# Optimization experiments

Hardware: AMD Instinct MI355X
Metric: run time of the kernel (lower is better)

Reference implementation:

```python
import math
import jax, jax.numpy as jnp
import numpy as np

N, L, D, H = 2, 2048, 1024, 16
DK = D // H  # 64


def setup_inputs() -> dict:
    key = jax.random.key(0)
    k1, k2, k3, k4, k5 = jax.random.split(key, 5)
    scale = 1.0 / math.sqrt(D)
    return {
        "values": jax.random.normal(k1, (N, L, D), dtype=jnp.float32),
        "keys": jax.random.normal(k2, (N, L, D), dtype=jnp.float32),
        "queries": jax.random.normal(k3, (N, L, D), dtype=jnp.float32),
        "fc_out_w": jax.random.normal(k4, (D, D), dtype=jnp.float32) * scale,
        "fc_out_b": jax.random.normal(k5, (D,), dtype=jnp.float32) * scale,
    }


def reference(values, keys, queries, fc_out_w, fc_out_b):
    n, q_len, _ = queries.shape
    k_len = keys.shape[1]
    v = values.reshape(n, k_len, H, DK)
    k = keys.reshape(n, k_len, H, DK)
    q = queries.reshape(n, q_len, H, DK)
    # NOTE: the original module never applies its per-head Linear layers (dead code),
    # and scales logits AFTER the QK einsum.
    energy = jnp.einsum('nqhd,nkhd->nhqk', q, k)  # [N,H,q,k]
    p_attn = jax.nn.softmax(energy / math.sqrt(DK), axis=3)
    attn = jnp.einsum('nhqk,nkhd->nqhd', p_attn, v).reshape(n, q_len, H * DK)
    # fc_out: torch Linear -> x @ W.T + b
    return attn @ fc_out_w.T + fc_out_b
```

## Files before the change

kernel.cpp:

```cpp
#include <hip/hip_runtime.h>
#include <hip/hip_bf16.h>

#define NBATCH 2
#define SEQ    2048
#define DMODEL 1024
#define NHEAD  16
#define DHEAD  64
#define NHTOT  (NBATCH*NHEAD)

typedef __attribute__((ext_vector_type(8)))  short          short8;
typedef __attribute__((ext_vector_type(4)))  float          f32x4;
typedef __attribute__((ext_vector_type(16))) float          f32x16;
typedef __attribute__((ext_vector_type(4)))  unsigned short ushort4v;

__device__ __forceinline__ unsigned short f2bf(float x) {
  union { __hip_bfloat16 b; unsigned short u; } c;
  c.b = __float2bfloat16(x);
  return c.u;
}

__device__ __forceinline__ unsigned int cvt_pk_bf16(float lo, float hi) {
  unsigned int r;
  asm("v_cvt_pk_bf16_f32 %0, %1, %2" : "=v"(r) : "v"(lo), "v"(hi));
  return r;
}

__device__ __forceinline__ void gl_lds16(const unsigned short* g, unsigned short* l) {
  __builtin_amdgcn_global_load_lds(
      (const __attribute__((address_space(1))) void*)g,
      (__attribute__((address_space(3))) void*)l, 16, 0, 0);
}

__global__ __launch_bounds__(256) void cvt_qk(const float* __restrict__ q,
                                              const float* __restrict__ k,
                                              unsigned short* __restrict__ qb,
                                              unsigned short* __restrict__ kb) {
  const float QSCALE = 0.125f * 1.44269504088896340736f;
  int e = (blockIdx.x * 256 + threadIdx.x) * 8;
  int n = e >> 21;
  int r = e & ((1 << 21) - 1);
  int l = r >> 10;
  int c = r & 1023;
  int h = c >> 6;
  int d = c & 63;
  size_t dst = ((size_t)(n * NHEAD + h) * SEQ + l) * DHEAD + d;
  float4 q0 = *reinterpret_cast<const float4*>(q + e);
  float4 q1 = *reinterpret_cast<const float4*>(q + e + 4);
  float4 k0 = *reinterpret_cast<const float4*>(k + e);
  float4 k1 = *reinterpret_cast<const float4*>(k + e + 4);
  union { unsigned short u[8]; short8 s; } qo, ko;
  qo.u[0]=f2bf(q0.x*QSCALE); qo.u[1]=f2bf(q0.y*QSCALE);
  qo.u[2]=f2bf(q0.z*QSCALE); qo.u[3]=f2bf(q0.w*QSCALE);
  qo.u[4]=f2bf(q1.x*QSCALE); qo.u[5]=f2bf(q1.y*QSCALE);
  qo.u[6]=f2bf(q1.z*QSCALE); qo.u[7]=f2bf(q1.w*QSCALE);
  ko.u[0]=f2bf(k0.x); ko.u[1]=f2bf(k0.y); ko.u[2]=f2bf(k0.z); ko.u[3]=f2bf(k0.w);
  ko.u[4]=f2bf(k1.x); ko.u[5]=f2bf(k1.y); ko.u[6]=f2bf(k1.z); ko.u[7]=f2bf(k1.w);
  *reinterpret_cast<short8*>(qb + dst) = qo.s;
  *reinterpret_cast<short8*>(kb + dst) = ko.s;
}

__global__ __launch_bounds__(256) void vtrans(const float* __restrict__ v,
                                              unsigned short* __restrict__ vt) {
  __shared__ __align__(16) unsigned short t[64][76];
  int bid = blockIdx.x;
  int nh = bid >> 5;
  int lt = bid & 31;
  int n = nh >> 4, h = nh & 15;
  int lbase = lt * 64;
  #pragma unroll
  for (int p = 0; p < 4; ++p) {
    int idx = p * 256 + threadIdx.x;
    int e = idx * 4;
    int l = e >> 6, d = e & 63;
    float4 x = *reinterpret_cast<const float4*>(
        v + ((size_t)n * SEQ + lbase + l) * DMODEL + h * DHEAD + d);
    ushort4v o;
    o.x = f2bf(x.x); o.y = f2bf(x.y); o.z = f2bf(x.z); o.w = f2bf(x.w);
    *reinterpret_cast<ushort4v*>(&t[l][d]) = o;
  }
  __syncthreads();
  #pragma unroll
  for (int p = 0; p < 4; ++p) {
    int idx = p * 256 + threadIdx.x;
    int d = idx >> 4, lq = (idx & 15) * 4;
    ushort4v o;
    o.x = t[lq + 0][d]; o.y = t[lq + 1][d];
    o.z = t[lq + 2][d]; o.w = t[lq + 3][d];
    *reinterpret_cast<ushort4v*>(
        vt + ((size_t)nh * DHEAD + d) * SEQ + lbase + lq) = o;
  }
}

__global__ __launch_bounds__(256) void cvt_w(const float* __restrict__ w,
                                             unsigned short* __restrict__ wb) {
  int e = (blockIdx.x * 256 + threadIdx.x) * 8;
  float4 w0 = *reinterpret_cast<const float4*>(w + e);
  float4 w1 = *reinterpret_cast<const float4*>(w + e + 4);
  union { unsigned short u[8]; short8 s; } wo;
  wo.u[0]=f2bf(w0.x); wo.u[1]=f2bf(w0.y); wo.u[2]=f2bf(w0.z); wo.u[3]=f2bf(w0.w);
  wo.u[4]=f2bf(w1.x); wo.u[5]=f2bf(w1.y); wo.u[6]=f2bf(w1.z); wo.u[7]=f2bf(w1.w);
  *reinterpret_cast<short8*>(wb + e) = wo.s;
}

__global__ __launch_bounds__(256, 2) void attn_fwd(const unsigned short* __restrict__ Qb,
                                                   const unsigned short* __restrict__ Kb,
                                                   const unsigned short* __restrict__ Vt,
                                                   unsigned short* __restrict__ Ab) {
  __shared__ __align__(16) unsigned short smem[3 * 8192];

  const int bid = blockIdx.x;
  const int nh = (bid & 7) * 4 + (bid >> 7);
  const int qt = (bid >> 3) & 15;
  const int tid  = threadIdx.x;
  const int wave = tid >> 6;
  const int lane = tid & 63;
  const int l31  = lane & 31;
  const int hi   = lane >> 5;

  const unsigned short* Kb_nh = Kb + (size_t)nh * SEQ * DHEAD;
  const unsigned short* Vt_nh = Vt + (size_t)nh * DHEAD * SEQ;

  short8 bq[4];
  {
    const unsigned short* Qrow =
        Qb + ((size_t)nh * SEQ + qt * 128 + wave * 32 + l31) * DHEAD + hi * 8;
    #pragma unroll
    for (int ds = 0; ds < 4; ++ds)
      bq[ds] = *reinterpret_cast<const short8*>(Qrow + ds * 16);
  }

  const short ONEB = (short)0x3F80;
  const short8 aones = {ONEB, ONEB, ONEB, ONEB, ONEB, ONEB, ONEB, ONEB};

  f32x16 acc[2], acc_l;
  #pragma unroll
  for (int r = 0; r < 16; ++r) { acc[0][r] = 0.f; acc[1][r] = 0.f; acc_l[r] = 0.f; }

  auto stage = [&](int t) {
    unsigned short* base = smem + (t % 3) * 8192;
    int kk = t * 64;
    #pragma unroll
    for (int j = 0; j < 2; ++j) {
      int c = j * 256 + tid;
      int row = c >> 3, cs = c & 7;
      int cg  = cs ^ (row & 7);
      int cb  = j * 256 + (tid & 192);
      gl_lds16(Kb_nh + (size_t)(kk + row) * DHEAD + cg * 8, base + cb * 8);
      gl_lds16(Vt_nh + (size_t)row * SEQ + kk + cg * 8,     base + 4096 + cb * 8);
    }
  };

  const int NT = SEQ / 64;
  stage(0);
  stage(1);

  for (int it = 0; it < NT; ++it) {
    if (it + 1 < NT) asm volatile("s_waitcnt vmcnt(4)" ::: "memory");
    else             asm volatile("s_waitcnt vmcnt(0)" ::: "memory");
    __builtin_amdgcn_s_barrier();
    if (it + 2 < NT) stage(it + 2);

    const unsigned short* kb = smem + (it % 3) * 8192;
    const unsigned short* vb = kb + 4096;

    f32x16 s[2];
    __builtin_amdgcn_s_setprio(1);
    #pragma unroll
    for (int kt = 0; kt < 2; ++kt) {
      #pragma unroll
      for (int r = 0; r < 16; ++r) s[kt][r] = 0.f;
      const int row = kt * 32 + l31;
      const int sw  = row & 7;
      const unsigned short* kr = kb + row * 64;
      #pragma unroll
      for (int ds = 0; ds < 4; ++ds) {
        short8 ak = *reinterpret_cast<const short8*>(kr + (((ds * 2 + hi) ^ sw) * 8));
        s[kt] = __builtin_amdgcn_mfma_f32_32x32x16_bf16(ak, bq[ds], s[kt], 0, 0, 0);
      }
    }
    __builtin_amdgcn_s_setprio(0);

    #pragma unroll
    for (int kt = 0; kt < 2; ++kt)
      #pragma unroll
      for (int r = 0; r < 16; ++r) s[kt][r] = exp2f(s[kt][r]);

    unsigned int pk[2][8];
    #pragma unroll
    for (int kt = 0; kt < 2; ++kt)
      #pragma unroll
      for (int i = 0; i < 8; ++i)
        pk[kt][i] = cvt_pk_bf16(s[kt][2 * i], s[kt][2 * i + 1]);

    short8 pfrag[4];
    #pragma unroll
    for (int ks = 0; ks < 4; ++ks) {
      const int t = ks >> 1, b = (ks & 1) * 4;
      unsigned int p0 = pk[t][b + 0], p2 = pk[t][b + 2];
      asm("v_permlane32_swap_b32 %0, %1" : "+v"(p0), "+v"(p2));
      unsigned int p1 = pk[t][b + 1], p3 = pk[t][b + 3];
      asm("v_permlane32_swap_b32 %0, %1" : "+v"(p1), "+v"(p3));
      union { unsigned int u[4]; short8 s8; } pu;
      pu.u[0] = p0; pu.u[1] = p1; pu.u[2] = p2; pu.u[3] = p3;
      pfrag[ks] = pu.s8;
    }

    __builtin_amdgcn_s_setprio(1);
    #pragma unroll
    for (int ks = 0; ks < 4; ++ks)
      acc_l = __builtin_amdgcn_mfma_f32_32x32x16_bf16(aones, pfrag[ks], acc_l, 0, 0, 0);
    #pragma unroll
    for (int dt = 0; dt < 2; ++dt) {
      const int row = dt * 32 + l31;
      const int sw  = row & 7;
      const unsigned short* vr = vb + row * 64;
      #pragma unroll
      for (int ks = 0; ks < 4; ++ks) {
        short8 av = *reinterpret_cast<const short8*>(vr + (((ks * 2 + hi) ^ sw) * 8));
        acc[dt] = __builtin_amdgcn_mfma_f32_32x32x16_bf16(av, pfrag[ks], acc[dt], 0, 0, 0);
      }
    }
    __builtin_amdgcn_s_setprio(0);
  }

  __syncthreads();

  unsigned short (*obuf)[32][80] = (unsigned short(*)[32][80])(&smem[0]);
  const float inv = 1.0f / acc_l[0];
  const int n = nh >> 4, h = nh & 15;
  #pragma unroll
  for (int dt = 0; dt < 2; ++dt)
    #pragma unroll
    for (int q4 = 0; q4 < 4; ++q4) {
      ushort4v pv;
      pv.x = f2bf(acc[dt][q4 * 4 + 0] * inv);
      pv.y = f2bf(acc[dt][q4 * 4 + 1] * inv);
      pv.z = f2bf(acc[dt][q4 * 4 + 2] * inv);
      pv.w = f2bf(acc[dt][q4 * 4 + 3] * inv);
      *reinterpret_cast<ushort4v*>(&obuf[wave][l31][dt * 32 + q4 * 8 + hi * 4]) = pv;
    }
  __syncthreads();
  #pragma unroll
  for (int rep = 0; rep < 4; ++rep) {
    int idx = rep * 256 + tid;
    int qi = idx >> 3, ch = idx & 7;
    int w = qi >> 5, qr = qi & 31;
    ushort4v v0 = *reinterpret_cast<const ushort4v*>(&obuf[w][qr][ch * 8]);
    ushort4v v1 = *reinterpret_cast<const ushort4v*>(&obuf[w][qr][ch * 8 + 4]);
    union { ushort4v hh[2]; short8 s; } vv;
    vv.hh[0] = v0; vv.hh[1] = v1;
    size_t orow = (size_t)n * SEQ + qt * 128 + qi;
    *reinterpret_cast<short8*>(Ab + orow * DMODEL + h * 64 + ch * 8) = vv.s;
  }
}

__global__ __launch_bounds__(256) void fc_gemm(const unsigned short* __restrict__ Ab,
                                               const unsigned short* __restrict__ Wb,
                                               const float* __restrict__ bias,
                                               float* __restrict__ out) {
  __shared__ __align__(16) unsigned short At[3][128 * 32];
  __shared__ __align__(16) unsigned short Bt[3][128 * 32];
  const int bid = blockIdx.x;
  const int bn = bid & 7;
  const int bm = bid >> 3;
  const int tid = threadIdx.x;
  const int wave = tid >> 6, lane = tid & 63;
  const int wr = wave >> 1, wc = wave & 1;
  const int l15 = lane & 15, l4 = lane >> 4;

  f32x4 acc[4][4];
  #pragma unroll
  for (int i = 0; i < 4; ++i)
    #pragma unroll
    for (int j = 0; j < 4; ++j) acc[i][j] = (f32x4){0.f, 0.f, 0.f, 0.f};

  auto stage = [&](int t) {
    int buf = t % 3, k0 = t * 32;
    #pragma unroll
    for (int j = 0; j < 2; ++j) {
      int c = j * 256 + tid;
      int row = c >> 2, cs = c & 3;
      int cg = cs ^ (row & 3);
      int cb = j * 256 + (tid & 192);
      gl_lds16(Ab + (size_t)(bm * 128 + row) * DMODEL + k0 + cg * 8, &At[buf][cb * 8]);
      gl_lds16(Wb + (size_t)(bn * 128 + row) * DMODEL + k0 + cg * 8, &Bt[buf][cb * 8]);
    }
  };

  const int NT = DMODEL / 32;
  stage(0);
  stage(1);

  for (int it = 0; it < NT; ++it) {
    if (it + 1 < NT) asm volatile("s_waitcnt vmcnt(4)" ::: "memory");
    else             asm volatile("s_waitcnt vmcnt(0)" ::: "memory");
    __builtin_amdgcn_s_barrier();
    if (it + 2 < NT) stage(it + 2);
    int cur = it % 3;

    short8 af[4], bf2[4];
    #pragma unroll
    for (int mt = 0; mt < 4; ++mt) {
      int row = wr * 64 + mt * 16 + l15;
      af[mt] = *reinterpret_cast<const short8*>(
          &At[cur][row * 32 + ((l4 ^ (row & 3)) * 8)]);
    }
    #pragma unroll
    for (int nt = 0; nt < 4; ++nt) {
      int row = wc * 64 + nt * 16 + l15;
      bf2[nt] = *reinterpret_cast<const short8*>(
          &Bt[cur][row * 32 + ((l4 ^ (row & 3)) * 8)]);
    }
    __builtin_amdgcn_s_setprio(1);
    #pragma unroll
    for (int mt = 0; mt < 4; ++mt)
      #pragma unroll
      for (int nt = 0; nt < 4; ++nt)
        acc[mt][nt] = __builtin_amdgcn_mfma_f32_16x16x32_bf16(af[mt], bf2[nt], acc[mt][nt], 0, 0, 0);
    __builtin_amdgcn_s_setprio(0);
  }

  #pragma unroll
  for (int mt = 0; mt < 4; ++mt)
    #pragma unroll
    for (int nt = 0; nt < 4; ++nt) {
      int col = bn * 128 + wc * 64 + nt * 16 + l15;
      float bv = bias[col];
      #pragma unroll
      for (int r = 0; r < 4; ++r) {
        int row = bm * 128 + wr * 64 + mt * 16 + l4 * 4 + r;
        out[(size_t)row * DMODEL + col] = acc[mt][nt][r] + bv;
      }
    }
}

extern "C" void kernel_launch(void* const* d_in, const int* in_sizes, int n_in,
                              void* d_out, int out_size, void* d_ws, size_t ws_size,
                              hipStream_t stream) {
  const float* values  = (const float*)d_in[0];
  const float* keys    = (const float*)d_in[1];
  const float* queries = (const float*)d_in[2];
  const float* fc_w    = (const float*)d_in[3];
  const float* fc_b    = (const float*)d_in[4];
  float* out = (float*)d_out;

  char* ws = (char*)d_ws;
  const size_t QKV_BYTES = (size_t)NHTOT * SEQ * DHEAD * 2;
  unsigned short* Qb = (unsigned short*)(ws);
  unsigned short* Kb = (unsigned short*)(ws + QKV_BYTES);
  unsigned short* Vt = (unsigned short*)(ws + 2 * QKV_BYTES);
  unsigned short* Wb = (unsigned short*)(ws + 3 * QKV_BYTES);
  unsigned short* Ab = (unsigned short*)(ws + 3 * QKV_BYTES + (size_t)DMODEL * DMODEL * 2);

  cvt_qk<<<2048, 256, 0, stream>>>(queries, keys, Qb, Kb);
  vtrans<<<1024, 256, 0, stream>>>(values, Vt);
  cvt_w<<<512, 256, 0, stream>>>(fc_w, Wb);
  attn_fwd<<<NHTOT * (SEQ / 128), 256, 0, stream>>>(Qb, Kb, Vt, Ab);
  fc_gemm<<<(NBATCH * SEQ / 128) * (DMODEL / 128), 256, 0, stream>>>(Ab, Wb, fc_b, out);
}
```

Baseline: 186.4 us.

## Split attention KV range across two blocks and merge partials; fuse prep kernels

Merges the three conversion kernels into one prep launch with block-range dispatch. The attention kernel now splits each (head, q-tile) KV sweep into two halves handled by separate blocks, doubling the grid to 1024 blocks with 4-per-CU occupancy and a 2-stage buffer. Each half writes fp32 partial accumulators and row sums to workspace, and the last-arriving block (via an atomic flag) adds them and normalizes. This targets underutilization from only 512 blocks, at the cost of partial-sum traffic, a memset, and shallower prefetch. The merge needs no max correction because the softmax runs without max subtraction.

Result: slower. 327.6 us (+75.8%).

```diff
diff --git a/kernel.cpp b/kernel.cpp
--- a/kernel.cpp
+++ b/kernel.cpp
@@ -31,86 +31,96 @@
       (__attribute__((address_space(3))) void*)l, 16, 0, 0);
 }
 
-__global__ __launch_bounds__(256) void cvt_qk(const float* __restrict__ q,
-                                              const float* __restrict__ k,
-                                              unsigned short* __restrict__ qb,
-                                              unsigned short* __restrict__ kb) {
-  const float QSCALE = 0.125f * 1.44269504088896340736f;
-  int e = (blockIdx.x * 256 + threadIdx.x) * 8;
-  int n = e >> 21;
-  int r = e & ((1 << 21) - 1);
-  int l = r >> 10;
-  int c = r & 1023;
-  int h = c >> 6;
-  int d = c & 63;
-  size_t dst = ((size_t)(n * NHEAD + h) * SEQ + l) * DHEAD + d;
-  float4 q0 = *reinterpret_cast<const float4*>(q + e);
-  float4 q1 = *reinterpret_cast<const float4*>(q + e + 4);
-  float4 k0 = *reinterpret_cast<const float4*>(k + e);
-  float4 k1 = *reinterpret_cast<const float4*>(k + e + 4);
-  union { unsigned short u[8]; short8 s; } qo, ko;
-  qo.u[0]=f2bf(q0.x*QSCALE); qo.u[1]=f2bf(q0.y*QSCALE);
-  qo.u[2]=f2bf(q0.z*QSCALE); qo.u[3]=f2bf(q0.w*QSCALE);
-  qo.u[4]=f2bf(q1.x*QSCALE); qo.u[5]=f2bf(q1.y*QSCALE);
-  qo.u[6]=f2bf(q1.z*QSCALE); qo.u[7]=f2bf(q1.w*QSCALE);
-  ko.u[0]=f2bf(k0.x); ko.u[1]=f2bf(k0.y); ko.u[2]=f2bf(k0.z); ko.u[3]=f2bf(k0.w);
-  ko.u[4]=f2bf(k1.x); ko.u[5]=f2bf(k1.y); ko.u[6]=f2bf(k1.z); ko.u[7]=f2bf(k1.w);
-  *reinterpret_cast<short8*>(qb + dst) = qo.s;
-  *reinterpret_cast<short8*>(kb + dst) = ko.s;
-}
-
-__global__ __launch_bounds__(256) void vtrans(const float* __restrict__ v,
-                                              unsigned short* __restrict__ vt) {
+__global__ __launch_bounds__(256) void prep(const float* __restrict__ v,
+                                            const float* __restrict__ k,
+                                            const float* __restrict__ q,
+                                            const float* __restrict__ w,
+                                            unsigned short* __restrict__ qb,
+                                            unsigned short* __restrict__ kb,
+                                            unsigned short* __restrict__ vt,
+                                            unsigned short* __restrict__ wb) {
   __shared__ __align__(16) unsigned short t[64][76];
-  int bid = blockIdx.x;
-  int nh = bid >> 5;
-  int lt = bid & 31;
-  int n = nh >> 4, h = nh & 15;
-  int lbase = lt * 64;
-  #pragma unroll
-  for (int p = 0; p < 4; ++p) {
-    int idx = p * 256 + threadIdx.x;
-    int e = idx * 4;
-    int l = e >> 6, d = e & 63;
-    float4 x = *reinterpret_cast<const float4*>(
-        v + ((size_t)n * SEQ + lbase + l) * DMODEL + h * DHEAD + d);
-    ushort4v o;
-    o.x = f2bf(x.x); o.y = f2bf(x.y); o.z = f2bf(x.z); o.w = f2bf(x.w);
-    *reinterpret_cast<ushort4v*>(&t[l][d]) = o;
+  const int b = blockIdx.x;
+  if (b < 2048) {
+    const float QSCALE = 0.125f * 1.44269504088896340736f;
+    int e = (b * 256 + threadIdx.x) * 8;
+    int n = e >> 21;
+    int r = e & ((1 << 21) - 1);
+    int l = r >> 10;
+    int c = r & 1023;
+    int h = c >> 6;
+    int d = c & 63;
+    size_t dst = ((size_t)(n * NHEAD + h) * SEQ + l) * DHEAD + d;
+    float4 q0 = *reinterpret_cast<const float4*>(q + e);
+    float4 q1 = *reinterpret_cast<const float4*>(q + e + 4);
+    float4 k0 = *reinterpret_cast<const float4*>(k + e);
+    float4 k1 = *reinterpret_cast<const float4*>(k + e + 4);
+    union { unsigned short u[8]; short8 s; } qo, ko;
+    qo.u[0]=f2bf(q0.x*QSCALE); qo.u[1]=f2bf(q0.y*QSCALE);
+    qo.u[2]=f2bf(q0.z*QSCALE); qo.u[3]=f2bf(q0.w*QSCALE);
+    qo.u[4]=f2bf(q1.x*QSCALE); qo.u[5]=f2bf(q1.y*QSCALE);
+    qo.u[6]=f2bf(q1.z*QSCALE); qo.u[7]=f2bf(q1.w*QSCALE);
+    ko.u[0]=f2bf(k0.x); ko.u[1]=f2bf(k0.y); ko.u[2]=f2bf(k0.z); ko.u[3]=f2bf(k0.w);
+    ko.u[4]=f2bf(k1.x); ko.u[5]=f2bf(k1.y); ko.u[6]=f2bf(k1.z); ko.u[7]=f2bf(k1.w);
+    *reinterpret_cast<short8*>(qb + dst) = qo.s;
+    *reinterpret_cast<short8*>(kb + dst) = ko.s;
+  } else if (b < 3072) {
+    int bid = b - 2048;
+    int nh = bid >> 5;
+    int lt = bid & 31;
+    int n = nh >> 4, h = nh & 15;
+    int lbase = lt * 64;
+    #pragma unroll
+    for (int p = 0; p < 4; ++p) {
+      int idx = p * 256 + threadIdx.x;
+      int e = idx * 4;
+      int l = e >> 6, d = e & 63;
+      float4 x = *reinterpret_cast<const float4*>(
+          v + ((size_t)n * SEQ + lbase + l) * DMODEL + h * DHEAD + d);
+      ushort4v o;
+      o.x = f2bf(x.x); o.y = f2bf(x.y); o.z = f2bf(x.z); o.w = f2bf(x.w);
+      *reinterpret_cast<ushort4v*>(&t[l][d]) = o;
+    }
+    __syncthreads();
+    #pragma unroll
+    for (int p = 0; p < 4; ++p) {
+      int idx = p * 256 + threadIdx.x;
+      int d = idx >> 4, lq = (idx & 15) * 4;
+      ushort4v o;
+      o.x = t[lq + 0][d]; o.y = t[lq + 1][d];
+      o.z = t[lq + 2][d]; o.w = t[lq + 3][d];
+      *reinterpret_cast<ushort4v*>(
+          vt + ((size_t)nh * DHEAD + d) * SEQ + lbase + lq) = o;
+    }
+  } else {
+    int e = ((b - 3072) * 256 + threadIdx.x) * 8;
+    float4 w0 = *reinterpret_cast<const float4*>(w + e);
+    float4 w1 = *reinterpret_cast<const float4*>(w + e + 4);
+    union { unsigned short u[8]; short8 s; } wo;
+    wo.u[0]=f2bf(w0.x); wo.u[1]=f2bf(w0.y); wo.u[2]=f2bf(w0.z); wo.u[3]=f2bf(w0.w);
+    wo.u[4]=f2bf(w1.x); wo.u[5]=f2bf(w1.y); wo.u[6]=f2bf(w1.z); wo.u[7]=f2bf(w1.w);
+    *reinterpret_cast<short8*>(wb + e) = wo.s;
   }
-  __syncthreads();
-  #pragma unroll
-  for (int p = 0; p < 4; ++p) {
-    int idx = p * 256 + threadIdx.x;
-    int d = idx >> 4, lq = (idx & 15) * 4;
-    ushort4v o;
-    o.x = t[lq + 0][d]; o.y = t[lq + 1][d];
-    o.z = t[lq + 2][d]; o.w = t[lq + 3][d];
-    *reinterpret_cast<ushort4v*>(
-        vt + ((size_t)nh * DHEAD + d) * SEQ + lbase + lq) = o;
-  }
-}
-
-__global__ __launch_bounds__(256) void cvt_w(const float* __restrict__ w,
-                                             unsigned short* __restrict__ wb) {
-  int e = (blockIdx.x * 256 + threadIdx.x) * 8;
-  float4 w0 = *reinterpret_cast<const float4*>(w + e);
-  float4 w1 = *reinterpret_cast<const float4*>(w + e + 4);
-  union { unsigned short u[8]; short8 s; } wo;
-  wo.u[0]=f2bf(w0.x); wo.u[1]=f2bf(w0.y); wo.u[2]=f2bf(w0.z); wo.u[3]=f2bf(w0.w);
-  wo.u[4]=f2bf(w1.x); wo.u[5]=f2bf(w1.y); wo.u[6]=f2bf(w1.z); wo.u[7]=f2bf(w1.w);
-  *reinterpret_cast<short8*>(wb + e) = wo.s;
-}
-
-__global__ __launch_bounds__(256, 2) void attn_fwd(const unsigned short* __restrict__ Qb,
+}
+
+__global__ __launch_bounds__(256, 4) void attn_fwd(const unsigned short* __restrict__ Qb,
                                                    const unsigned short* __restrict__ Kb,
                                                    const unsigned short* __restrict__ Vt,
-                                                   unsigned short* __restrict__ Ab) {
-  __shared__ __align__(16) unsigned short smem[3 * 8192];
-
-  const int bid = blockIdx.x;
-  const int nh = (bid & 7) * 4 + (bid >> 7);
-  const int qt = (bid >> 3) & 15;
+                                                   unsigned short* __restrict__ Ab,
+                                                   float* __restrict__ part,
+                                                   int* __restrict__ flags) {
+  __shared__ __align__(16) unsigned short smem[2 * 8192];
+  __shared__ int s_old;
+
+  const int bid  = blockIdx.x;
+  const int xcd  = bid & 7;
+  const int j    = bid >> 3;
+  const int nhl  = j >> 5;
+  const int qt   = (j >> 1) & 15;
+  const int half = j & 1;
+  const int nh   = xcd * 4 + nhl;
+  const int pair = nh * 16 + qt;
+
   const int tid  = threadIdx.x;
   const int wave = tid >> 6;
   const int lane = tid & 63;
@@ -136,31 +146,31 @@
   #pragma unroll
   for (int r = 0; r < 16; ++r) { acc[0][r] = 0.f; acc[1][r] = 0.f; acc_l[r] = 0.f; }
 
-  auto stage = [&](int t) {
-    unsigned short* base = smem + (t % 3) * 8192;
-    int kk = t * 64;
-    #pragma unroll
-    for (int j = 0; j < 2; ++j) {
-      int c = j * 256 + tid;
+  const int NT = SEQ / 64 / 2;
+  const int t0 = half * NT;
+
+  auto stage = [&](int lit) {
+    unsigned short* base = smem + (lit & 1) * 8192;
+    int kk = (t0 + lit) * 64;
+    #pragma unroll
+    for (int jj = 0; jj < 2; ++jj) {
+      int c = jj * 256 + tid;
       int row = c >> 3, cs = c & 7;
       int cg  = cs ^ (row & 7);
-      int cb  = j * 256 + (tid & 192);
+      int cb  = jj * 256 + (tid & 192);
       gl_lds16(Kb_nh + (size_t)(kk + row) * DHEAD + cg * 8, base + cb * 8);
       gl_lds16(Vt_nh + (size_t)row * SEQ + kk + cg * 8,     base + 4096 + cb * 8);
     }
   };
 
-  const int NT = SEQ / 64;
   stage(0);
-  stage(1);
-
-  for (int it = 0; it < NT; ++it) {
-    if (it + 1 < NT) asm volatile("s_waitcnt vmcnt(4)" ::: "memory");
-    else             asm volatile("s_waitcnt vmcnt(0)" ::: "memory");
+
+  for (int lit = 0; lit < NT; ++lit) {
+    asm volatile("s_waitcnt vmcnt(0)" ::: "memory");
     __builtin_amdgcn_s_barrier();
-    if (it + 2 < NT) stage(it + 2);
-
-    const unsigned short* kb = smem + (it % 3) * 8192;
+    if (lit + 1 < NT) stage(lit + 1);
+
+    const unsigned short* kb = smem + (lit & 1) * 8192;
     const unsigned short* vb = kb + 4096;
 
     f32x16 s[2];
@@ -195,10 +205,10 @@
     short8 pfrag[4];
     #pragma unroll
     for (int ks = 0; ks < 4; ++ks) {
-      const int t = ks >> 1, b = (ks & 1) * 4;
-      unsigned int p0 = pk[t][b + 0], p2 = pk[t][b + 2];
+      const int tt = ks >> 1, b = (ks & 1) * 4;
+      unsigned int p0 = pk[tt][b + 0], p2 = pk[tt][b + 2];
       asm("v_permlane32_swap_b32 %0, %1" : "+v"(p0), "+v"(p2));
-      unsigned int p1 = pk[t][b + 1], p3 = pk[t][b + 3];
+      unsigned int p1 = pk[tt][b + 1], p3 = pk[tt][b + 3];
       asm("v_permlane32_swap_b32 %0, %1" : "+v"(p1), "+v"(p3));
       union { unsigned int u[4]; short8 s8; } pu;
       pu.u[0] = p0; pu.u[1] = p1; pu.u[2] = p2; pu.u[3] = p3;
@@ -223,10 +233,38 @@
     __builtin_amdgcn_s_setprio(0);
   }
 
+  float* pb = part + (size_t)(pair * 2 + half) * 65 * 128;
+  #pragma unroll
+  for (int dt = 0; dt < 2; ++dt)
+    #pragma unroll
+    for (int r = 0; r < 16; ++r) {
+      int d = dt * 32 + (r & 3) + 8 * (r >> 2) + 4 * hi;
+      pb[d * 128 + wave * 32 + l31] = acc[dt][r];
+    }
+  if (hi == 0) pb[64 * 128 + wave * 32 + l31] = acc_l[0];
+
+  __threadfence();
+  if (tid == 0)
+    s_old = __hip_atomic_fetch_add(&flags[pair], 1, __ATOMIC_ACQ_REL,
+                                   __HIP_MEMORY_SCOPE_AGENT);
   __syncthreads();
-
+  if (s_old == 0) return;
+
+  const float* po = part + (size_t)(pair * 2 + (1 - half)) * 65 * 128;
+  #pragma unroll
+  for (int dt = 0; dt < 2; ++dt)
+    #pragma unroll
+    for (int r = 0; r < 16; ++r) {
+      int d = dt * 32 + (r & 3) + 8 * (r >> 2) + 4 * hi;
+      acc[dt][r] += __hip_atomic_load(&po[d * 128 + wave * 32 + l31],
+                                      __ATOMIC_RELAXED, __HIP_MEMORY_SCOPE_AGENT);
+    }
+  float lsum = acc_l[0] + __hip_atomic_load(&po[64 * 128 + wave * 32 + l31],
+                                            __ATOMIC_RELAXED, __HIP_MEMORY_SCOPE_AGENT);
+  const float inv = 1.0f / lsum;
+
+  __syncthreads();
   unsigned short (*obuf)[32][80] = (unsigned short(*)[32][80])(&smem[0]);
-  const float inv = 1.0f / acc_l[0];
   const int n = nh >> 4, h = nh & 15;
   #pragma unroll
   for (int dt = 0; dt < 2; ++dt)
@@ -351,10 +389,13 @@
   unsigned short* Vt = (unsigned short*)(ws + 2 * QKV_BYTES);
   unsigned short* Wb = (unsigned short*)(ws + 3 * QKV_BYTES);
   unsigned short* Ab = (unsigned short*)(ws + 3 * QKV_BYTES + (size_t)DMODEL * DMODEL * 2);
-
-  cvt_qk<<<2048, 256, 0, stream>>>(queries, keys, Qb, Kb);
-  vtrans<<<1024, 256, 0, stream>>>(values, Vt);
-  cvt_w<<<512, 256, 0, stream>>>(fc_w, Wb);
-  attn_fwd<<<NHTOT * (SEQ / 128), 256, 0, stream>>>(Qb, Kb, Vt, Ab);
+  char* after_ab = ws + 3 * QKV_BYTES + (size_t)DMODEL * DMODEL * 2 +
+                   (size_t)NBATCH * SEQ * DMODEL * 2;
+  int*   flags = (int*)after_ab;
+  float* part  = (float*)(after_ab + 4096);
+
+  prep<<<3584, 256, 0, stream>>>(values, keys, queries, fc_w, Qb, Kb, Vt, Wb);
+  hipMemsetAsync(flags, 0, 512 * sizeof(int), stream);
+  attn_fwd<<<1024, 256, 0, stream>>>(Qb, Kb, Vt, Ab, part, flags);
   fc_gemm<<<(NBATCH * SEQ / 128) * (DMODEL / 128), 256, 0, stream>>>(Ab, Wb, fc_b, out);
 }
```
